# Performance work log

Measured on AMD Instinct MI355X. Metric: run time of the kernel, lower is better.

Reference implementation:

```python
import jax, jax.numpy as jnp
import numpy as np

N = 20000   # mesh vertices
B = 8       # batch
F = 64      # in_channels
K = 6       # Chebyshev order
OUT = 64    # out_channels
NNZ = 320000  # nonzeros in sparse Laplacian (avg degree 16)


def setup_inputs() -> dict:
    key = jax.random.key(0)
    ks = jax.random.split(key, 6)
    x = jax.random.normal(ks[0], (B, N, F), dtype=jnp.float32)
    lap_rows = jax.random.randint(ks[1], (NNZ,), 0, N, dtype=jnp.int32)
    lap_cols = jax.random.randint(ks[2], (NNZ,), 0, N, dtype=jnp.int32)
    lap_vals = jax.random.normal(ks[3], (NNZ,), dtype=jnp.float32) * 0.05
    # fc: Linear(K*F, OUT), xavier_normal weight, zero bias
    W = jax.random.normal(ks[4], (OUT, K * F), dtype=jnp.float32) * float(np.sqrt(2.0 / (K * F + OUT)))
    b = jnp.zeros((OUT,), dtype=jnp.float32)
    return {"x": x, "lap_rows": lap_rows, "lap_cols": lap_cols,
            "lap_vals": lap_vals, "W": W, "b": b}


def reference(x, lap_rows, lap_cols, lap_vals, W, b):
    Bd, Nd, Fd = x.shape

    def spmm(v):  # sparse [N,N] @ dense [N, B*F] via COO gather + segment_sum
        return jax.ops.segment_sum(lap_vals[:, None] * v[lap_cols], lap_rows,
                                   num_segments=Nd)

    x0 = jnp.transpose(x, (1, 0, 2)).reshape(Nd, Bd * Fd)  # [N, B*F]
    outs = [x0]
    if K > 1:
        tx1 = spmm(x0)
        outs.append(tx1)
        tx0 = x0
        for _ in range(2, K):  # Chebyshev recurrence T_k = 2 L T_{k-1} - T_{k-2}
            tx2 = 2.0 * spmm(tx1) - tx0
            outs.append(tx2)
            tx0, tx1 = tx1, tx2
    out = jnp.concatenate([o.reshape(Nd, Bd, Fd) for o in outs], axis=2)  # [N,B,K*F]
    out = out.reshape(Nd * Bd, K * Fd) @ W.T + b  # dense fc
    return jnp.transpose(out.reshape(Nd, Bd, -1), (1, 0, 2))  # [B,N,OUT]
```

## Files before the change

kernel.cpp:

```cpp
#include <hip/hip_runtime.h>

#define N_V  20000
#define B_   8
#define F_   64
#define K_   6
#define OUT_ 64
#define NNZ_ 320000
#define BF   512
#define NBUK N_V
#define SCANB 20
#define EPAD (NNZ_ + N_V * 7)

typedef unsigned short ushort_t;
typedef unsigned int   uint_t;

using frag_ab = __attribute__((ext_vector_type(8))) short;
using frag_cd = __attribute__((ext_vector_type(4))) float;

__device__ __forceinline__ ushort_t f2bf(float f) {
    uint_t u = __float_as_uint(f);
    u += 0x7FFFu + ((u >> 16) & 1u);
    return (ushort_t)(u >> 16);
}
__device__ __forceinline__ uint_t pack2(float lo, float hi) {
    return (uint_t)f2bf(lo) | ((uint_t)f2bf(hi) << 16);
}
__device__ __forceinline__ float bf2f(ushort_t u) {
    return __uint_as_float((uint_t)u << 16);
}


__global__ void hist_kernel(const int* __restrict__ rows, int* __restrict__ counts) {
    int e = blockIdx.x * 256 + threadIdx.x;
    if (e < NNZ_) atomicAdd(&counts[rows[e]], 1);
}

__global__ __launch_bounds__(1024) void scan1(const int* __restrict__ counts,
                                              int* __restrict__ incl, int* __restrict__ bsum) {
    __shared__ int buf[1024];
    int tid = threadIdx.x;
    int i = blockIdx.x * 1024 + tid;
    int c = (i < NBUK) ? ((counts[i] + 7) & ~7) : 0;
    buf[tid] = c;
    __syncthreads();
    for (int off = 1; off < 1024; off <<= 1) {
        int t = buf[tid];
        int add = (tid >= off) ? buf[tid - off] : 0;
        __syncthreads();
        buf[tid] = t + add;
        __syncthreads();
    }
    if (i < NBUK) incl[i] = buf[tid];
    if (tid == 1023) bsum[blockIdx.x] = buf[1023];
}

__global__ __launch_bounds__(256) void scan2(int* __restrict__ bsum) {
    __shared__ int buf[256];
    int tid = threadIdx.x;
    int c = (tid < SCANB) ? bsum[tid] : 0;
    buf[tid] = c;
    __syncthreads();
    for (int off = 1; off < 256; off <<= 1) {
        int t = buf[tid];
        int add = (tid >= off) ? buf[tid - off] : 0;
        __syncthreads();
        buf[tid] = t + add;
        __syncthreads();
    }
    if (tid < SCANB) bsum[tid] = buf[tid] - c;
}

__global__ __launch_bounds__(1024) void scan3(const int* __restrict__ counts,
                                              const int* __restrict__ bsum,
                                              int* __restrict__ bp, int* __restrict__ cursor) {
    int tid = threadIdx.x;
    int i = blockIdx.x * 1024 + tid;
    if (i < NBUK) {
        int pc = (counts[i] + 7) & ~7;
        int p = bsum[blockIdx.x] + cursor[i];
        bp[i + 1] = p;
        cursor[i] = p - pc;
    }
    if (i == 0) bp[0] = 0;
}

__global__ void scatter_kernel(const int* __restrict__ rows, const int* __restrict__ cols,
                               const float* __restrict__ vals, int* __restrict__ cursor,
                               int2* __restrict__ edges) {
    int e = blockIdx.x * 256 + threadIdx.x;
    if (e < NNZ_) {
        int pos = atomicAdd(&cursor[rows[e]], 1);
        edges[pos] = make_int2(cols[e], __float_as_int(vals[e]));
    }
}

__global__ void prep_kernel(const float* __restrict__ x, uint_t* __restrict__ X0,
                            const float* __restrict__ W, ushort_t* __restrict__ Wfrag) {
    int blk = blockIdx.x;
    if (blk < 20000) {
        int idx = blk * 256 + threadIdx.x;
        int f2 = idx & 31;
        int b  = (idx >> 5) & 7;
        int n  = idx >> 8;
        float2 v = *(const float2*)&x[((size_t)b * N_V + n) * F_ + f2 * 2];
        X0[n * 256 + b * 32 + f2] = pack2(v.x, v.y);
    } else {
        int idx = (blk - 20000) * 256 + threadIdx.x;
        if (idx < 12 * 4 * 64 * 8) {
            int j    = idx & 7;
            int lane = (idx >> 3) & 63;
            int ct   = (idx >> 9) & 3;
            int s    = idx >> 11;
            int o     = ct * 16 + (lane & 15);
            int kglob = s * 32 + ((lane >> 4) & 3) * 8 + j;
            Wfrag[idx] = f2bf(W[o * (K_ * F_) + kglob]);
        }
    }
}

template <bool RECUR>
__global__ __launch_bounds__(256) void cheb_row(const int* __restrict__ bp,
                                                const int2* __restrict__ edges,
                                                const ushort_t* __restrict__ Tprev,
                                                const ushort_t* __restrict__ Tpp,
                                                ushort_t* __restrict__ Tout) {
    const int wave = __builtin_amdgcn_readfirstlane(threadIdx.x >> 6);
    const int lane = threadIdx.x & 63;
    const int c    = blockIdx.x & 7;
    const int row  = ((blockIdx.x >> 3) << 2) + wave;

    const int st = bp[row];
    const int en = bp[row + 1];
    const ushort_t* Tp = Tprev + (c << 6) + lane;

    float a0 = 0.f, a1 = 0.f;
    for (int j = st; j < en; j += 8) {
        const int4* e4 = (const int4*)(edges + j);
        int4 E0 = e4[0], E1 = e4[1], E2 = e4[2], E3 = e4[3];
        const int c0 = __builtin_amdgcn_readfirstlane(E0.x);
        const int c1 = __builtin_amdgcn_readfirstlane(E0.z);
        const int c2 = __builtin_amdgcn_readfirstlane(E1.x);
        const int c3 = __builtin_amdgcn_readfirstlane(E1.z);
        const int c4 = __builtin_amdgcn_readfirstlane(E2.x);
        const int c5 = __builtin_amdgcn_readfirstlane(E2.z);
        const int c6 = __builtin_amdgcn_readfirstlane(E3.x);
        const int c7 = __builtin_amdgcn_readfirstlane(E3.z);
        const float v0 = __int_as_float(__builtin_amdgcn_readfirstlane(E0.y));
        const float v1 = __int_as_float(__builtin_amdgcn_readfirstlane(E0.w));
        const float v2 = __int_as_float(__builtin_amdgcn_readfirstlane(E1.y));
        const float v3 = __int_as_float(__builtin_amdgcn_readfirstlane(E1.w));
        const float v4 = __int_as_float(__builtin_amdgcn_readfirstlane(E2.y));
        const float v5 = __int_as_float(__builtin_amdgcn_readfirstlane(E2.w));
        const float v6 = __int_as_float(__builtin_amdgcn_readfirstlane(E3.y));
        const float v7 = __int_as_float(__builtin_amdgcn_readfirstlane(E3.w));

        ushort_t t0 = Tp[(size_t)c0 << 9];
        ushort_t t1 = Tp[(size_t)c1 << 9];
        ushort_t t2 = Tp[(size_t)c2 << 9];
        ushort_t t3 = Tp[(size_t)c3 << 9];
        ushort_t t4 = Tp[(size_t)c4 << 9];
        ushort_t t5 = Tp[(size_t)c5 << 9];
        ushort_t t6 = Tp[(size_t)c6 << 9];
        ushort_t t7 = Tp[(size_t)c7 << 9];

        a0 = fmaf(v0, bf2f(t0), a0);
        a1 = fmaf(v1, bf2f(t1), a1);
        a0 = fmaf(v2, bf2f(t2), a0);
        a1 = fmaf(v3, bf2f(t3), a1);
        a0 = fmaf(v4, bf2f(t4), a0);
        a1 = fmaf(v5, bf2f(t5), a1);
        a0 = fmaf(v6, bf2f(t6), a0);
        a1 = fmaf(v7, bf2f(t7), a1);
    }

    float res = a0 + a1;
    const size_t oidx = (size_t)row * BF + (c << 6) + lane;
    if (RECUR) {
        res = fmaf(2.f, res, -bf2f(Tpp[oidx]));
    }
    Tout[oidx] = f2bf(res);
}

__global__ __launch_bounds__(256) void fc_mfma(const ushort_t* __restrict__ X0,
                                               const ushort_t* __restrict__ T1,
                                               const ushort_t* __restrict__ T2,
                                               const ushort_t* __restrict__ T3,
                                               const ushort_t* __restrict__ T4,
                                               const ushort_t* __restrict__ T5,
                                               const ushort_t* __restrict__ Wfrag,
                                               const float* __restrict__ bias,
                                               float* __restrict__ out) {
    const int wave = threadIdx.x >> 6, lane = threadIdx.x & 63;
    const int quad = lane >> 4, col = lane & 15;
    const int tb = blockIdx.x * 128 + wave * 32;
    const int r0 = tb + col, r1 = tb + 16 + col;
    const ushort_t* Tbuf[6] = {X0, T1, T2, T3, T4, T5};

    frag_cd acc0[4], acc1[4];
#pragma unroll
    for (int ct = 0; ct < 4; ++ct) {
        acc0[ct] = (frag_cd){0.f, 0.f, 0.f, 0.f};
        acc1[ct] = (frag_cd){0.f, 0.f, 0.f, 0.f};
    }

#pragma unroll
    for (int s = 0; s < 12; ++s) {
        const int f0 = (s & 1) * 32 + quad * 8;
        frag_ab fa0 = *(const frag_ab*)(Tbuf[s >> 1] + (size_t)r0 * F_ + f0);
        frag_ab fa1 = *(const frag_ab*)(Tbuf[s >> 1] + (size_t)r1 * F_ + f0);
#pragma unroll
        for (int ct = 0; ct < 4; ++ct) {
            frag_ab bfr = *(const frag_ab*)(Wfrag + (((s * 4 + ct) * 64 + lane) << 3));
            acc0[ct] = __builtin_amdgcn_mfma_f32_16x16x32_bf16(fa0, bfr, acc0[ct], 0, 0, 0);
            acc1[ct] = __builtin_amdgcn_mfma_f32_16x16x32_bf16(fa1, bfr, acc1[ct], 0, 0, 0);
        }
    }

#pragma unroll
    for (int ct = 0; ct < 4; ++ct) {
        const int o = ct * 16 + col;
        const float bv = bias[o];
#pragma unroll
        for (int reg = 0; reg < 4; ++reg) {
            int ra = tb + quad * 4 + reg;
            int rb = ra + 16;
            out[(size_t)(ra & 7) * N_V * OUT_ + (size_t)(ra >> 3) * OUT_ + o] = acc0[ct][reg] + bv;
            out[(size_t)(rb & 7) * N_V * OUT_ + (size_t)(rb >> 3) * OUT_ + o] = acc1[ct][reg] + bv;
        }
    }
}


extern "C" void kernel_launch(void* const* d_in, const int* in_sizes, int n_in,
                              void* d_out, int out_size, void* d_ws, size_t ws_size,
                              hipStream_t stream) {
    const float* x    = (const float*)d_in[0];
    const int*   rows = (const int*)  d_in[1];
    const int*   cols = (const int*)  d_in[2];
    const float* vals = (const float*)d_in[3];
    const float* W    = (const float*)d_in[4];
    const float* bias = (const float*)d_in[5];
    float* out = (float*)d_out;

    const size_t TSZ = (size_t)N_V * BF;
    ushort_t* T1 = (ushort_t*)d_ws;
    ushort_t* T2 = T1 + TSZ;
    ushort_t* T3 = T2 + TSZ;
    ushort_t* T4 = T3 + TSZ;
    ushort_t* T5 = T4 + TSZ;
    ushort_t* X0 = T5 + TSZ;
    ushort_t* Wfrag = X0 + TSZ;
    int* counts    = (int*)(Wfrag + 24576);
    int* bp        = counts + NBUK;
    int* cursor    = bp + NBUK + 64;
    int* bsum      = cursor + NBUK;
    int2* edges    = (int2*)(bsum + 256);

    hipMemsetAsync(counts, 0, NBUK * sizeof(int), stream);
    hipMemsetAsync(edges, 0, (size_t)EPAD * sizeof(int2), stream);
    hist_kernel<<<(NNZ_ + 255) / 256, 256, 0, stream>>>(rows, counts);
    scan1<<<SCANB, 1024, 0, stream>>>(counts, cursor, bsum);
    scan2<<<1, 256, 0, stream>>>(bsum);
    scan3<<<SCANB, 1024, 0, stream>>>(counts, bsum, bp, cursor);
    scatter_kernel<<<(NNZ_ + 255) / 256, 256, 0, stream>>>(rows, cols, vals, cursor, edges);
    prep_kernel<<<20096, 256, 0, stream>>>(x, (uint_t*)X0, W, Wfrag);

    const int chebGrid = (N_V / 4) * 8;
    cheb_row<false><<<chebGrid, 256, 0, stream>>>(bp, edges, X0, nullptr, T1);
    cheb_row<true ><<<chebGrid, 256, 0, stream>>>(bp, edges, T1, X0, T2);
    cheb_row<true ><<<chebGrid, 256, 0, stream>>>(bp, edges, T2, T1, T3);
    cheb_row<true ><<<chebGrid, 256, 0, stream>>>(bp, edges, T3, T2, T4);
    cheb_row<true ><<<chebGrid, 256, 0, stream>>>(bp, edges, T4, T3, T5);

    fc_mfma<<<(N_V * B_) / 128, 256, 0, stream>>>(X0, T1, T2, T3, T4, T5, Wfrag, bias, out);
}
```

Before: 453.0 us.

## Process two rows per wave with 4-wide feature vectors and edge-group split

Rewrites the Chebyshev SpMM kernel so each wave handles two adjacent rows. Lanes are split into 4 edge groups of 16 lanes, and each lane loads 4 bf16 features (8 bytes) per gathered neighbor instead of one 2-byte value. Per-row edge padding rises from 8 to 16 so a 16-edge step stays within the padded region, and partial sums are reduced across groups with shuffles. The aim is wider gather loads and fewer waves, at the cost of more zero padding work, extra padded-edge memory and a cross-lane reduction.

```diff
diff --git a/kernel.cpp b/kernel.cpp
--- a/kernel.cpp
+++ b/kernel.cpp
@@ -9,7 +9,7 @@
 #define BF   512
 #define NBUK N_V
 #define SCANB 20
-#define EPAD (NNZ_ + N_V * 7)
+#define EPAD (NNZ_ + N_V * 15)
 
 typedef unsigned short ushort_t;
 typedef unsigned int   uint_t;
@@ -25,8 +25,9 @@
 __device__ __forceinline__ uint_t pack2(float lo, float hi) {
     return (uint_t)f2bf(lo) | ((uint_t)f2bf(hi) << 16);
 }
-__device__ __forceinline__ float bf2f(ushort_t u) {
-    return __uint_as_float((uint_t)u << 16);
+__device__ __forceinline__ void unpack2(uint_t u, float& lo, float& hi) {
+    lo = __uint_as_float(u << 16);
+    hi = __uint_as_float(u & 0xFFFF0000u);
 }
 
 
@@ -40,7 +41,7 @@
     __shared__ int buf[1024];
     int tid = threadIdx.x;
     int i = blockIdx.x * 1024 + tid;
-    int c = (i < NBUK) ? ((counts[i] + 7) & ~7) : 0;
+    int c = (i < NBUK) ? ((counts[i] + 15) & ~15) : 0;
     buf[tid] = c;
     __syncthreads();
     for (int off = 1; off < 1024; off <<= 1) {
@@ -76,7 +77,7 @@
     int tid = threadIdx.x;
     int i = blockIdx.x * 1024 + tid;
     if (i < NBUK) {
-        int pc = (counts[i] + 7) & ~7;
+        int pc = (counts[i] + 15) & ~15;
         int p = bsum[blockIdx.x] + cursor[i];
         bp[i + 1] = p;
         cursor[i] = p - pc;
@@ -119,66 +120,99 @@
 }
 
 template <bool RECUR>
-__global__ __launch_bounds__(256) void cheb_row(const int* __restrict__ bp,
-                                                const int2* __restrict__ edges,
-                                                const ushort_t* __restrict__ Tprev,
-                                                const ushort_t* __restrict__ Tpp,
-                                                ushort_t* __restrict__ Tout) {
-    const int wave = __builtin_amdgcn_readfirstlane(threadIdx.x >> 6);
-    const int lane = threadIdx.x & 63;
+__global__ __launch_bounds__(256) void cheb_row2(const int* __restrict__ bp,
+                                                 const int2* __restrict__ edges,
+                                                 const ushort_t* __restrict__ Tprev,
+                                                 const ushort_t* __restrict__ Tpp,
+                                                 ushort_t* __restrict__ Tout) {
+    const int wave = threadIdx.x >> 6, lane = threadIdx.x & 63;
     const int c    = blockIdx.x & 7;
-    const int row  = ((blockIdx.x >> 3) << 2) + wave;
-
-    const int st = bp[row];
-    const int en = bp[row + 1];
-    const ushort_t* Tp = Tprev + (c << 6) + lane;
-
-    float a0 = 0.f, a1 = 0.f;
-    for (int j = st; j < en; j += 8) {
-        const int4* e4 = (const int4*)(edges + j);
-        int4 E0 = e4[0], E1 = e4[1], E2 = e4[2], E3 = e4[3];
-        const int c0 = __builtin_amdgcn_readfirstlane(E0.x);
-        const int c1 = __builtin_amdgcn_readfirstlane(E0.z);
-        const int c2 = __builtin_amdgcn_readfirstlane(E1.x);
-        const int c3 = __builtin_amdgcn_readfirstlane(E1.z);
-        const int c4 = __builtin_amdgcn_readfirstlane(E2.x);
-        const int c5 = __builtin_amdgcn_readfirstlane(E2.z);
-        const int c6 = __builtin_amdgcn_readfirstlane(E3.x);
-        const int c7 = __builtin_amdgcn_readfirstlane(E3.z);
-        const float v0 = __int_as_float(__builtin_amdgcn_readfirstlane(E0.y));
-        const float v1 = __int_as_float(__builtin_amdgcn_readfirstlane(E0.w));
-        const float v2 = __int_as_float(__builtin_amdgcn_readfirstlane(E1.y));
-        const float v3 = __int_as_float(__builtin_amdgcn_readfirstlane(E1.w));
-        const float v4 = __int_as_float(__builtin_amdgcn_readfirstlane(E2.y));
-        const float v5 = __int_as_float(__builtin_amdgcn_readfirstlane(E2.w));
-        const float v6 = __int_as_float(__builtin_amdgcn_readfirstlane(E3.y));
-        const float v7 = __int_as_float(__builtin_amdgcn_readfirstlane(E3.w));
-
-        ushort_t t0 = Tp[(size_t)c0 << 9];
-        ushort_t t1 = Tp[(size_t)c1 << 9];
-        ushort_t t2 = Tp[(size_t)c2 << 9];
-        ushort_t t3 = Tp[(size_t)c3 << 9];
-        ushort_t t4 = Tp[(size_t)c4 << 9];
-        ushort_t t5 = Tp[(size_t)c5 << 9];
-        ushort_t t6 = Tp[(size_t)c6 << 9];
-        ushort_t t7 = Tp[(size_t)c7 << 9];
-
-        a0 = fmaf(v0, bf2f(t0), a0);
-        a1 = fmaf(v1, bf2f(t1), a1);
-        a0 = fmaf(v2, bf2f(t2), a0);
-        a1 = fmaf(v3, bf2f(t3), a1);
-        a0 = fmaf(v4, bf2f(t4), a0);
-        a1 = fmaf(v5, bf2f(t5), a1);
-        a0 = fmaf(v6, bf2f(t6), a0);
-        a1 = fmaf(v7, bf2f(t7), a1);
-    }
-
-    float res = a0 + a1;
-    const size_t oidx = (size_t)row * BF + (c << 6) + lane;
-    if (RECUR) {
-        res = fmaf(2.f, res, -bf2f(Tpp[oidx]));
-    }
-    Tout[oidx] = f2bf(res);
+    const int pair = (blockIdx.x >> 3) * 4 + wave;
+    const int r0   = pair * 2;
+    const int g    = lane >> 4;
+    const int f4   = (lane & 15) << 2;
+
+    const int st  = bp[r0];
+    const int mid = bp[r0 + 1];
+    const int en  = bp[r0 + 2];
+
+    const ushort_t* Tb = Tprev + (c << 6) + f4;
+    const int2*    eb  = edges + g * 4;
+
+    float a0 = 0.f, a1 = 0.f, a2 = 0.f, a3 = 0.f;
+    float b0 = 0.f, b1 = 0.f, b2 = 0.f, b3 = 0.f;
+
+    for (int j = st; j < en; j += 16) {
+        const int4* ep = (const int4*)(eb + j);
+        int4 Ea = ep[0];
+        int4 Eb = ep[1];
+        uint2 u0 = *(const uint2*)(Tb + ((size_t)Ea.x << 9));
+        uint2 u1 = *(const uint2*)(Tb + ((size_t)Ea.z << 9));
+        uint2 u2 = *(const uint2*)(Tb + ((size_t)Eb.x << 9));
+        uint2 u3 = *(const uint2*)(Tb + ((size_t)Eb.z << 9));
+        const float v0 = __int_as_float(Ea.y);
+        const float v1 = __int_as_float(Ea.w);
+        const float v2 = __int_as_float(Eb.y);
+        const float v3 = __int_as_float(Eb.w);
+        float e0, e1, e2, e3;
+        if (j < mid) {
+            unpack2(u0.x, e0, e1); unpack2(u0.y, e2, e3);
+            a0 = fmaf(v0, e0, a0); a1 = fmaf(v0, e1, a1);
+            a2 = fmaf(v0, e2, a2); a3 = fmaf(v0, e3, a3);
+            unpack2(u1.x, e0, e1); unpack2(u1.y, e2, e3);
+            a0 = fmaf(v1, e0, a0); a1 = fmaf(v1, e1, a1);
+            a2 = fmaf(v1, e2, a2); a3 = fmaf(v1, e3, a3);
+            unpack2(u2.x, e0, e1); unpack2(u2.y, e2, e3);
+            a0 = fmaf(v2, e0, a0); a1 = fmaf(v2, e1, a1);
+            a2 = fmaf(v2, e2, a2); a3 = fmaf(v2, e3, a3);
+            unpack2(u3.x, e0, e1); unpack2(u3.y, e2, e3);
+            a0 = fmaf(v3, e0, a0); a1 = fmaf(v3, e1, a1);
+            a2 = fmaf(v3, e2, a2); a3 = fmaf(v3, e3, a3);
+        } else {
+            unpack2(u0.x, e0, e1); unpack2(u0.y, e2, e3);
+            b0 = fmaf(v0, e0, b0); b1 = fmaf(v0, e1, b1);
+            b2 = fmaf(v0, e2, b2); b3 = fmaf(v0, e3, b3);
+            unpack2(u1.x, e0, e1); unpack2(u1.y, e2, e3);
+            b0 = fmaf(v1, e0, b0); b1 = fmaf(v1, e1, b1);
+            b2 = fmaf(v1, e2, b2); b3 = fmaf(v1, e3, b3);
+            unpack2(u2.x, e0, e1); unpack2(u2.y, e2, e3);
+            b0 = fmaf(v2, e0, b0); b1 = fmaf(v2, e1, b1);
+            b2 = fmaf(v2, e2, b2); b3 = fmaf(v2, e3, b3);
+            unpack2(u3.x, e0, e1); unpack2(u3.y, e2, e3);
+            b0 = fmaf(v3, e0, b0); b1 = fmaf(v3, e1, b1);
+            b2 = fmaf(v3, e2, b2); b3 = fmaf(v3, e3, b3);
+        }
+    }
+
+    a0 += __shfl_xor(a0, 16, 64); a0 += __shfl_xor(a0, 32, 64);
+    a1 += __shfl_xor(a1, 16, 64); a1 += __shfl_xor(a1, 32, 64);
+    a2 += __shfl_xor(a2, 16, 64); a2 += __shfl_xor(a2, 32, 64);
+    a3 += __shfl_xor(a3, 16, 64); a3 += __shfl_xor(a3, 32, 64);
+    b0 += __shfl_xor(b0, 16, 64); b0 += __shfl_xor(b0, 32, 64);
+    b1 += __shfl_xor(b1, 16, 64); b1 += __shfl_xor(b1, 32, 64);
+    b2 += __shfl_xor(b2, 16, 64); b2 += __shfl_xor(b2, 32, 64);
+    b3 += __shfl_xor(b3, 16, 64); b3 += __shfl_xor(b3, 32, 64);
+
+    if (lane < 32) {
+        float s0 = (lane < 16) ? a0 : b0;
+        float s1 = (lane < 16) ? a1 : b1;
+        float s2 = (lane < 16) ? a2 : b2;
+        float s3 = (lane < 16) ? a3 : b3;
+        const size_t o = (size_t)(r0 + (lane >> 4)) * BF + (c << 6) + f4;
+        if (RECUR) {
+            uint2 up = *(const uint2*)(Tpp + o);
+            float p0, p1, p2, p3;
+            unpack2(up.x, p0, p1); unpack2(up.y, p2, p3);
+            s0 = fmaf(2.f, s0, -p0);
+            s1 = fmaf(2.f, s1, -p1);
+            s2 = fmaf(2.f, s2, -p2);
+            s3 = fmaf(2.f, s3, -p3);
+        }
+        uint2 st2;
+        st2.x = pack2(s0, s1);
+        st2.y = pack2(s2, s3);
+        *(uint2*)(Tout + o) = st2;
+    }
 }
 
 __global__ __launch_bounds__(256) void fc_mfma(const ushort_t* __restrict__ X0,
@@ -265,12 +299,12 @@
     scatter_kernel<<<(NNZ_ + 255) / 256, 256, 0, stream>>>(rows, cols, vals, cursor, edges);
     prep_kernel<<<20096, 256, 0, stream>>>(x, (uint_t*)X0, W, Wfrag);
 
-    const int chebGrid = (N_V / 4) * 8;
-    cheb_row<false><<<chebGrid, 256, 0, stream>>>(bp, edges, X0, nullptr, T1);
-    cheb_row<true ><<<chebGrid, 256, 0, stream>>>(bp, edges, T1, X0, T2);
-    cheb_row<true ><<<chebGrid, 256, 0, stream>>>(bp, edges, T2, T1, T3);
-    cheb_row<true ><<<chebGrid, 256, 0, stream>>>(bp, edges, T3, T2, T4);
-    cheb_row<true ><<<chebGrid, 256, 0, stream>>>(bp, edges, T4, T3, T5);
+    const int chebGrid = 2500 * 8;
+    cheb_row2<false><<<chebGrid, 256, 0, stream>>>(bp, edges, X0, nullptr, T1);
+    cheb_row2<true ><<<chebGrid, 256, 0, stream>>>(bp, edges, T1, X0, T2);
+    cheb_row2<true ><<<chebGrid, 256, 0, stream>>>(bp, edges, T2, T1, T3);
+    cheb_row2<true ><<<chebGrid, 256, 0, stream>>>(bp, edges, T3, T2, T4);
+    cheb_row2<true ><<<chebGrid, 256, 0, stream>>>(bp, edges, T4, T3, T5);
 
     fc_mfma<<<(N_V * B_) / 128, 256, 0, stream>>>(X0, T1, T2, T3, T4, T5, Wfrag, bias, out);
 }
```

New measurement: 420.3 us. 7.2% less time.

## Restructure Chebyshev SpMM: wave handles two rows with 8-edge lanes and 16-byte gathers

Applied to the files above, without the earlier changes.

Rewrites the sparse Chebyshev step so each wave covers two adjacent rows of a 64-column chunk. The 64 lanes are split into 8 edge slots of 8 lanes, and each lane gathers 8 bf16 features with a single 16-byte load instead of one 2-byte load per lane. Edge and gather loads are software-pipelined two iterations ahead, and partial sums are combined with cross-lane shuffles before 16 lanes write vectorized outputs. This targets the small scalar gathers and per-edge uniform-register broadcasts, at the cost of extra shuffle reductions and per-edge row-select branching.

```diff
diff --git a/kernel.cpp b/kernel.cpp
--- a/kernel.cpp
+++ b/kernel.cpp
@@ -25,8 +25,9 @@
 __device__ __forceinline__ uint_t pack2(float lo, float hi) {
     return (uint_t)f2bf(lo) | ((uint_t)f2bf(hi) << 16);
 }
-__device__ __forceinline__ float bf2f(ushort_t u) {
-    return __uint_as_float((uint_t)u << 16);
+__device__ __forceinline__ void unpack2(uint_t u, float& lo, float& hi) {
+    lo = __uint_as_float(u << 16);
+    hi = __uint_as_float(u & 0xFFFF0000u);
 }
 
 
@@ -119,66 +120,95 @@
 }
 
 template <bool RECUR>
-__global__ __launch_bounds__(256) void cheb_row(const int* __restrict__ bp,
-                                                const int2* __restrict__ edges,
-                                                const ushort_t* __restrict__ Tprev,
-                                                const ushort_t* __restrict__ Tpp,
-                                                ushort_t* __restrict__ Tout) {
-    const int wave = __builtin_amdgcn_readfirstlane(threadIdx.x >> 6);
-    const int lane = threadIdx.x & 63;
+__global__ __launch_bounds__(256) void cheb_row8(const int* __restrict__ bp,
+                                                 const int2* __restrict__ edges,
+                                                 const ushort_t* __restrict__ Tprev,
+                                                 const ushort_t* __restrict__ Tpp,
+                                                 ushort_t* __restrict__ Tout) {
+    const int wave = threadIdx.x >> 6, lane = threadIdx.x & 63;
     const int c    = blockIdx.x & 7;
-    const int row  = ((blockIdx.x >> 3) << 2) + wave;
-
-    const int st = bp[row];
-    const int en = bp[row + 1];
-    const ushort_t* Tp = Tprev + (c << 6) + lane;
-
-    float a0 = 0.f, a1 = 0.f;
-    for (int j = st; j < en; j += 8) {
-        const int4* e4 = (const int4*)(edges + j);
-        int4 E0 = e4[0], E1 = e4[1], E2 = e4[2], E3 = e4[3];
-        const int c0 = __builtin_amdgcn_readfirstlane(E0.x);
-        const int c1 = __builtin_amdgcn_readfirstlane(E0.z);
-        const int c2 = __builtin_amdgcn_readfirstlane(E1.x);
-        const int c3 = __builtin_amdgcn_readfirstlane(E1.z);
-        const int c4 = __builtin_amdgcn_readfirstlane(E2.x);
-        const int c5 = __builtin_amdgcn_readfirstlane(E2.z);
-        const int c6 = __builtin_amdgcn_readfirstlane(E3.x);
-        const int c7 = __builtin_amdgcn_readfirstlane(E3.z);
-        const float v0 = __int_as_float(__builtin_amdgcn_readfirstlane(E0.y));
-        const float v1 = __int_as_float(__builtin_amdgcn_readfirstlane(E0.w));
-        const float v2 = __int_as_float(__builtin_amdgcn_readfirstlane(E1.y));
-        const float v3 = __int_as_float(__builtin_amdgcn_readfirstlane(E1.w));
-        const float v4 = __int_as_float(__builtin_amdgcn_readfirstlane(E2.y));
-        const float v5 = __int_as_float(__builtin_amdgcn_readfirstlane(E2.w));
-        const float v6 = __int_as_float(__builtin_amdgcn_readfirstlane(E3.y));
-        const float v7 = __int_as_float(__builtin_amdgcn_readfirstlane(E3.w));
-
-        ushort_t t0 = Tp[(size_t)c0 << 9];
-        ushort_t t1 = Tp[(size_t)c1 << 9];
-        ushort_t t2 = Tp[(size_t)c2 << 9];
-        ushort_t t3 = Tp[(size_t)c3 << 9];
-        ushort_t t4 = Tp[(size_t)c4 << 9];
-        ushort_t t5 = Tp[(size_t)c5 << 9];
-        ushort_t t6 = Tp[(size_t)c6 << 9];
-        ushort_t t7 = Tp[(size_t)c7 << 9];
-
-        a0 = fmaf(v0, bf2f(t0), a0);
-        a1 = fmaf(v1, bf2f(t1), a1);
-        a0 = fmaf(v2, bf2f(t2), a0);
-        a1 = fmaf(v3, bf2f(t3), a1);
-        a0 = fmaf(v4, bf2f(t4), a0);
-        a1 = fmaf(v5, bf2f(t5), a1);
-        a0 = fmaf(v6, bf2f(t6), a0);
-        a1 = fmaf(v7, bf2f(t7), a1);
-    }
-
-    float res = a0 + a1;
-    const size_t oidx = (size_t)row * BF + (c << 6) + lane;
-    if (RECUR) {
-        res = fmaf(2.f, res, -bf2f(Tpp[oidx]));
-    }
-    Tout[oidx] = f2bf(res);
+    const int pair = (blockIdx.x >> 3) * 4 + wave;
+    const int r0   = pair * 2;
+    const int sub  = lane >> 3;
+    const int f8   = (lane & 7) << 3;
+
+    const int st  = bp[r0];
+    const int mid = bp[r0 + 1];
+    const int en  = bp[r0 + 2];
+
+    const ushort_t* Tb = Tprev + (c << 6) + f8;
+    const int2*    eb  = edges + sub;
+
+    float aA0 = 0.f, aA1 = 0.f, aA2 = 0.f, aA3 = 0.f,
+          aA4 = 0.f, aA5 = 0.f, aA6 = 0.f, aA7 = 0.f;
+    float aB0 = 0.f, aB1 = 0.f, aB2 = 0.f, aB3 = 0.f,
+          aB4 = 0.f, aB5 = 0.f, aB6 = 0.f, aB7 = 0.f;
+
+    if (st < en) {
+        const int lim = en - 8;
+        int2 E0 = eb[st];
+        int2 E1 = eb[min(st + 8, lim)];
+        int2 E2 = eb[min(st + 16, lim)];
+        uint4 G0 = *(const uint4*)(Tb + ((size_t)(uint_t)E0.x << 9));
+        uint4 G1 = *(const uint4*)(Tb + ((size_t)(uint_t)E1.x << 9));
+        float v0 = __int_as_float(E0.y);
+        float v1 = __int_as_float(E1.y);
+
+        for (int j = st; j < en; j += 8) {
+            uint4 Gn = *(const uint4*)(Tb + ((size_t)(uint_t)E2.x << 9));
+            float vn = __int_as_float(E2.y);
+            int2 En = eb[min(j + 24, lim)];
+            float e0, e1, e2, e3, e4, e5, e6, e7;
+            unpack2(G0.x, e0, e1); unpack2(G0.y, e2, e3);
+            unpack2(G0.z, e4, e5); unpack2(G0.w, e6, e7);
+            if (j < mid) {
+                aA0 = fmaf(v0, e0, aA0); aA1 = fmaf(v0, e1, aA1);
+                aA2 = fmaf(v0, e2, aA2); aA3 = fmaf(v0, e3, aA3);
+                aA4 = fmaf(v0, e4, aA4); aA5 = fmaf(v0, e5, aA5);
+                aA6 = fmaf(v0, e6, aA6); aA7 = fmaf(v0, e7, aA7);
+            } else {
+                aB0 = fmaf(v0, e0, aB0); aB1 = fmaf(v0, e1, aB1);
+                aB2 = fmaf(v0, e2, aB2); aB3 = fmaf(v0, e3, aB3);
+                aB4 = fmaf(v0, e4, aB4); aB5 = fmaf(v0, e5, aB5);
+                aB6 = fmaf(v0, e6, aB6); aB7 = fmaf(v0, e7, aB7);
+            }
+            G0 = G1; v0 = v1; G1 = Gn; v1 = vn; E2 = En;
+        }
+    }
+
+#define RED(x) x += __shfl_xor(x, 8, 64); x += __shfl_xor(x, 16, 64); x += __shfl_xor(x, 32, 64)
+    RED(aA0); RED(aA1); RED(aA2); RED(aA3); RED(aA4); RED(aA5); RED(aA6); RED(aA7);
+    RED(aB0); RED(aB1); RED(aB2); RED(aB3); RED(aB4); RED(aB5); RED(aB6); RED(aB7);
+#undef RED
+
+    if (lane < 16) {
+        const int isB = lane >> 3;
+        float s0 = isB ? aB0 : aA0;
+        float s1 = isB ? aB1 : aA1;
+        float s2 = isB ? aB2 : aA2;
+        float s3 = isB ? aB3 : aA3;
+        float s4 = isB ? aB4 : aA4;
+        float s5 = isB ? aB5 : aA5;
+        float s6 = isB ? aB6 : aA6;
+        float s7 = isB ? aB7 : aA7;
+        const size_t o = (size_t)(r0 + isB) * BF + (c << 6) + f8;
+        if (RECUR) {
+            uint4 up = *(const uint4*)(Tpp + o);
+            float p0, p1, p2, p3, p4, p5, p6, p7;
+            unpack2(up.x, p0, p1); unpack2(up.y, p2, p3);
+            unpack2(up.z, p4, p5); unpack2(up.w, p6, p7);
+            s0 = fmaf(2.f, s0, -p0); s1 = fmaf(2.f, s1, -p1);
+            s2 = fmaf(2.f, s2, -p2); s3 = fmaf(2.f, s3, -p3);
+            s4 = fmaf(2.f, s4, -p4); s5 = fmaf(2.f, s5, -p5);
+            s6 = fmaf(2.f, s6, -p6); s7 = fmaf(2.f, s7, -p7);
+        }
+        uint4 st4;
+        st4.x = pack2(s0, s1);
+        st4.y = pack2(s2, s3);
+        st4.z = pack2(s4, s5);
+        st4.w = pack2(s6, s7);
+        *(uint4*)(Tout + o) = st4;
+    }
 }
 
 __global__ __launch_bounds__(256) void fc_mfma(const ushort_t* __restrict__ X0,
@@ -265,12 +295,12 @@
     scatter_kernel<<<(NNZ_ + 255) / 256, 256, 0, stream>>>(rows, cols, vals, cursor, edges);
     prep_kernel<<<20096, 256, 0, stream>>>(x, (uint_t*)X0, W, Wfrag);
 
-    const int chebGrid = (N_V / 4) * 8;
-    cheb_row<false><<<chebGrid, 256, 0, stream>>>(bp, edges, X0, nullptr, T1);
-    cheb_row<true ><<<chebGrid, 256, 0, stream>>>(bp, edges, T1, X0, T2);
-    cheb_row<true ><<<chebGrid, 256, 0, stream>>>(bp, edges, T2, T1, T3);
-    cheb_row<true ><<<chebGrid, 256, 0, stream>>>(bp, edges, T3, T2, T4);
-    cheb_row<true ><<<chebGrid, 256, 0, stream>>>(bp, edges, T4, T3, T5);
+    const int chebGrid = 2500 * 8;
+    cheb_row8<false><<<chebGrid, 256, 0, stream>>>(bp, edges, X0, nullptr, T1);
+    cheb_row8<true ><<<chebGrid, 256, 0, stream>>>(bp, edges, T1, X0, T2);
+    cheb_row8<true ><<<chebGrid, 256, 0, stream>>>(bp, edges, T2, T1, T3);
+    cheb_row8<true ><<<chebGrid, 256, 0, stream>>>(bp, edges, T3, T2, T4);
+    cheb_row8<true ><<<chebGrid, 256, 0, stream>>>(bp, edges, T4, T3, T5);
 
     fc_mfma<<<(N_V * B_) / 128, 256, 0, stream>>>(X0, T1, T2, T3, T4, T5, Wfrag, bias, out);
 }
```

Result: faster. 423.5 us (-6.5%).

## Restructure Chebyshev SpMM to 16-byte gathers over row pairs, merge scan kernels

Applied to the files above, without the earlier changes.

The SpMM kernel now has each wave handle four rows as two pairs. Its 8 edge-subgroups each gather 16-byte bf16 vectors, with prefetch of the next edges and gathers. Cross-lane shuffle reductions combine the subgroup sums. This replaces the old scheme of one 2-byte gather per lane per edge, and aims to raise memory-level parallelism and cut instruction count per edge. The three scan kernels are merged into a single-block scan, and the two memsets are merged into one. The cost is more registers, shuffle overhead, and load imbalance between paired rows.

```diff
diff --git a/kernel.cpp b/kernel.cpp
--- a/kernel.cpp
+++ b/kernel.cpp
@@ -8,7 +8,6 @@
 #define NNZ_ 320000
 #define BF   512
 #define NBUK N_V
-#define SCANB 20
 #define EPAD (NNZ_ + N_V * 7)
 
 typedef unsigned short ushort_t;
@@ -25,8 +24,9 @@
 __device__ __forceinline__ uint_t pack2(float lo, float hi) {
     return (uint_t)f2bf(lo) | ((uint_t)f2bf(hi) << 16);
 }
-__device__ __forceinline__ float bf2f(ushort_t u) {
-    return __uint_as_float((uint_t)u << 16);
+__device__ __forceinline__ void unpack2(uint_t u, float& lo, float& hi) {
+    lo = __uint_as_float(u << 16);
+    hi = __uint_as_float(u & 0xFFFF0000u);
 }
 
 
@@ -35,13 +35,22 @@
     if (e < NNZ_) atomicAdd(&counts[rows[e]], 1);
 }
 
-__global__ __launch_bounds__(1024) void scan1(const int* __restrict__ counts,
-                                              int* __restrict__ incl, int* __restrict__ bsum) {
+__global__ __launch_bounds__(1024) void scan_all(const int* __restrict__ counts,
+                                                 int* __restrict__ bp,
+                                                 int* __restrict__ cursor) {
     __shared__ int buf[1024];
-    int tid = threadIdx.x;
-    int i = blockIdx.x * 1024 + tid;
-    int c = (i < NBUK) ? ((counts[i] + 7) & ~7) : 0;
-    buf[tid] = c;
+    const int tid = threadIdx.x;
+    int loc[20];
+    int s = 0;
+    if (tid < 1000) {
+        const int base = tid * 20;
+#pragma unroll
+        for (int k = 0; k < 20; ++k) {
+            loc[k] = s;
+            s += (counts[base + k] + 7) & ~7;
+        }
+    }
+    buf[tid] = s;
     __syncthreads();
     for (int off = 1; off < 1024; off <<= 1) {
         int t = buf[tid];
@@ -50,38 +59,17 @@
         buf[tid] = t + add;
         __syncthreads();
     }
-    if (i < NBUK) incl[i] = buf[tid];
-    if (tid == 1023) bsum[blockIdx.x] = buf[1023];
-}
-
-__global__ __launch_bounds__(256) void scan2(int* __restrict__ bsum) {
-    __shared__ int buf[256];
-    int tid = threadIdx.x;
-    int c = (tid < SCANB) ? bsum[tid] : 0;
-    buf[tid] = c;
-    __syncthreads();
-    for (int off = 1; off < 256; off <<= 1) {
-        int t = buf[tid];
-        int add = (tid >= off) ? buf[tid - off] : 0;
-        __syncthreads();
-        buf[tid] = t + add;
-        __syncthreads();
-    }
-    if (tid < SCANB) bsum[tid] = buf[tid] - c;
-}
-
-__global__ __launch_bounds__(1024) void scan3(const int* __restrict__ counts,
-                                              const int* __restrict__ bsum,
-                                              int* __restrict__ bp, int* __restrict__ cursor) {
-    int tid = threadIdx.x;
-    int i = blockIdx.x * 1024 + tid;
-    if (i < NBUK) {
-        int pc = (counts[i] + 7) & ~7;
-        int p = bsum[blockIdx.x] + cursor[i];
-        bp[i + 1] = p;
-        cursor[i] = p - pc;
-    }
-    if (i == 0) bp[0] = 0;
+    const int excl = buf[tid] - s;
+    if (tid < 1000) {
+        const int base = tid * 20;
+#pragma unroll
+        for (int k = 0; k < 20; ++k) {
+            const int p = excl + loc[k];
+            bp[base + k] = p;
+            cursor[base + k] = p;
+        }
+    }
+    if (tid == 1023) bp[NBUK] = buf[1023];
 }
 
 __global__ void scatter_kernel(const int* __restrict__ rows, const int* __restrict__ cols,
@@ -118,67 +106,123 @@
     }
 }
 
+#define CONS(Gv, vv, isA, accA, accB)                                          \
+    {                                                                          \
+        float e_[8];                                                           \
+        unpack2(Gv.x, e_[0], e_[1]); unpack2(Gv.y, e_[2], e_[3]);              \
+        unpack2(Gv.z, e_[4], e_[5]); unpack2(Gv.w, e_[6], e_[7]);              \
+        if (isA) {                                                             \
+            _Pragma("unroll")                                                  \
+            for (int i_ = 0; i_ < 8; ++i_) accA[i_] = fmaf(vv, e_[i_], accA[i_]); \
+        } else {                                                               \
+            _Pragma("unroll")                                                  \
+            for (int i_ = 0; i_ < 8; ++i_) accB[i_] = fmaf(vv, e_[i_], accB[i_]); \
+        }                                                                      \
+    }
+
 template <bool RECUR>
-__global__ __launch_bounds__(256) void cheb_row(const int* __restrict__ bp,
-                                                const int2* __restrict__ edges,
-                                                const ushort_t* __restrict__ Tprev,
-                                                const ushort_t* __restrict__ Tpp,
-                                                ushort_t* __restrict__ Tout) {
-    const int wave = __builtin_amdgcn_readfirstlane(threadIdx.x >> 6);
-    const int lane = threadIdx.x & 63;
+__global__ __launch_bounds__(256) void cheb_quad(const int* __restrict__ bp,
+                                                 const int2* __restrict__ edges,
+                                                 const ushort_t* __restrict__ Tprev,
+                                                 const ushort_t* __restrict__ Tpp,
+                                                 ushort_t* __restrict__ Tout) {
+    const int wave = threadIdx.x >> 6, lane = threadIdx.x & 63;
     const int c    = blockIdx.x & 7;
-    const int row  = ((blockIdx.x >> 3) << 2) + wave;
-
-    const int st = bp[row];
-    const int en = bp[row + 1];
-    const ushort_t* Tp = Tprev + (c << 6) + lane;
-
-    float a0 = 0.f, a1 = 0.f;
-    for (int j = st; j < en; j += 8) {
-        const int4* e4 = (const int4*)(edges + j);
-        int4 E0 = e4[0], E1 = e4[1], E2 = e4[2], E3 = e4[3];
-        const int c0 = __builtin_amdgcn_readfirstlane(E0.x);
-        const int c1 = __builtin_amdgcn_readfirstlane(E0.z);
-        const int c2 = __builtin_amdgcn_readfirstlane(E1.x);
-        const int c3 = __builtin_amdgcn_readfirstlane(E1.z);
-        const int c4 = __builtin_amdgcn_readfirstlane(E2.x);
-        const int c5 = __builtin_amdgcn_readfirstlane(E2.z);
-        const int c6 = __builtin_amdgcn_readfirstlane(E3.x);
-        const int c7 = __builtin_amdgcn_readfirstlane(E3.z);
-        const float v0 = __int_as_float(__builtin_amdgcn_readfirstlane(E0.y));
-        const float v1 = __int_as_float(__builtin_amdgcn_readfirstlane(E0.w));
-        const float v2 = __int_as_float(__builtin_amdgcn_readfirstlane(E1.y));
-        const float v3 = __int_as_float(__builtin_amdgcn_readfirstlane(E1.w));
-        const float v4 = __int_as_float(__builtin_amdgcn_readfirstlane(E2.y));
-        const float v5 = __int_as_float(__builtin_amdgcn_readfirstlane(E2.w));
-        const float v6 = __int_as_float(__builtin_amdgcn_readfirstlane(E3.y));
-        const float v7 = __int_as_float(__builtin_amdgcn_readfirstlane(E3.w));
-
-        ushort_t t0 = Tp[(size_t)c0 << 9];
-        ushort_t t1 = Tp[(size_t)c1 << 9];
-        ushort_t t2 = Tp[(size_t)c2 << 9];
-        ushort_t t3 = Tp[(size_t)c3 << 9];
-        ushort_t t4 = Tp[(size_t)c4 << 9];
-        ushort_t t5 = Tp[(size_t)c5 << 9];
-        ushort_t t6 = Tp[(size_t)c6 << 9];
-        ushort_t t7 = Tp[(size_t)c7 << 9];
-
-        a0 = fmaf(v0, bf2f(t0), a0);
-        a1 = fmaf(v1, bf2f(t1), a1);
-        a0 = fmaf(v2, bf2f(t2), a0);
-        a1 = fmaf(v3, bf2f(t3), a1);
-        a0 = fmaf(v4, bf2f(t4), a0);
-        a1 = fmaf(v5, bf2f(t5), a1);
-        a0 = fmaf(v6, bf2f(t6), a0);
-        a1 = fmaf(v7, bf2f(t7), a1);
-    }
-
-    float res = a0 + a1;
-    const size_t oidx = (size_t)row * BF + (c << 6) + lane;
-    if (RECUR) {
-        res = fmaf(2.f, res, -bf2f(Tpp[oidx]));
-    }
-    Tout[oidx] = f2bf(res);
+    const int grp  = (blockIdx.x >> 3) * 4 + wave;
+    const int r0   = grp * 4;
+    const int sub  = lane >> 3;
+    const int f8   = (lane & 7) << 3;
+
+    int bpv = bp[r0 + min(lane, 4)];
+    const int st0  = __builtin_amdgcn_readfirstlane(__shfl(bpv, 0, 64));
+    const int mid0 = __builtin_amdgcn_readfirstlane(__shfl(bpv, 1, 64));
+    const int en0  = __builtin_amdgcn_readfirstlane(__shfl(bpv, 2, 64));
+    const int mid1 = __builtin_amdgcn_readfirstlane(__shfl(bpv, 3, 64));
+    const int en1  = __builtin_amdgcn_readfirstlane(__shfl(bpv, 4, 64));
+    const int st1  = en0;
+
+    const int n0 = (en0 - st0) >> 3;
+    const int n1 = (en1 - st1) >> 3;
+    const int maxit = max(n0, n1);
+
+    const ushort_t* Tb = Tprev + (c << 6) + f8;
+    const int2*     eb = edges + sub;
+
+    float accA0[8], accB0[8], accA1[8], accB1[8];
+#pragma unroll
+    for (int i = 0; i < 8; ++i) { accA0[i] = 0.f; accB0[i] = 0.f; accA1[i] = 0.f; accB1[i] = 0.f; }
+
+    if (maxit > 0) {
+        const int safe0 = (n0 > 0) ? st0 : 0;
+        const int safe1 = (n1 > 0) ? st1 : 0;
+        const int last0 = safe0 + 8 * (max(n0, 1) - 1);
+        const int last1 = safe1 + 8 * (max(n1, 1) - 1);
+
+        int a0 = safe0, a1 = safe1;
+        int2 E0a = eb[a0];
+        int2 E1a = eb[a1];
+        int2 E0n = eb[min(safe0 + 8, last0)];
+        int2 E1n = eb[min(safe1 + 8, last1)];
+        uint4 G0 = *(const uint4*)(Tb + ((size_t)(uint_t)E0a.x << 9));
+        uint4 G1 = *(const uint4*)(Tb + ((size_t)(uint_t)E1a.x << 9));
+        float v0 = (n0 > 0) ? __int_as_float(E0a.y) : 0.f;
+        float v1 = (n1 > 0) ? __int_as_float(E1a.y) : 0.f;
+
+        for (int it = 0; it < maxit; ++it) {
+            uint4 Gn0 = *(const uint4*)(Tb + ((size_t)(uint_t)E0n.x << 9));
+            uint4 Gn1 = *(const uint4*)(Tb + ((size_t)(uint_t)E1n.x << 9));
+            const float vn0 = (it + 1 < n0) ? __int_as_float(E0n.y) : 0.f;
+            const float vn1 = (it + 1 < n1) ? __int_as_float(E1n.y) : 0.f;
+            int2 E0t = eb[min(a0 + 16, last0)];
+            int2 E1t = eb[min(a1 + 16, last1)];
+            CONS(G0, v0, (a0 < mid0), accA0, accB0);
+            CONS(G1, v1, (a1 < mid1), accA1, accB1);
+            G0 = Gn0; v0 = vn0; G1 = Gn1; v1 = vn1;
+            E0n = E0t; E1n = E1t;
+            a0 = min(a0 + 8, last0);
+            a1 = min(a1 + 8, last1);
+        }
+    }
+
+#pragma unroll
+    for (int i = 0; i < 8; ++i) {
+        accA0[i] += __shfl_xor(accA0[i], 8, 64); accA0[i] += __shfl_xor(accA0[i], 16, 64); accA0[i] += __shfl_xor(accA0[i], 32, 64);
+        accB0[i] += __shfl_xor(accB0[i], 8, 64); accB0[i] += __shfl_xor(accB0[i], 16, 64); accB0[i] += __shfl_xor(accB0[i], 32, 64);
+        accA1[i] += __shfl_xor(accA1[i], 8, 64); accA1[i] += __shfl_xor(accA1[i], 16, 64); accA1[i] += __shfl_xor(accA1[i], 32, 64);
+        accB1[i] += __shfl_xor(accB1[i], 8, 64); accB1[i] += __shfl_xor(accB1[i], 16, 64); accB1[i] += __shfl_xor(accB1[i], 32, 64);
+    }
+
+    if (lane < 16) {
+        const int isB = lane >> 3;
+        float s0[8], s1[8];
+#pragma unroll
+        for (int i = 0; i < 8; ++i) {
+            s0[i] = isB ? accB0[i] : accA0[i];
+            s1[i] = isB ? accB1[i] : accA1[i];
+        }
+        const size_t o0 = (size_t)(r0 + isB)     * BF + (c << 6) + f8;
+        const size_t o1 = (size_t)(r0 + 2 + isB) * BF + (c << 6) + f8;
+        if (RECUR) {
+            uint4 up0 = *(const uint4*)(Tpp + o0);
+            uint4 up1 = *(const uint4*)(Tpp + o1);
+            float p[8];
+            unpack2(up0.x, p[0], p[1]); unpack2(up0.y, p[2], p[3]);
+            unpack2(up0.z, p[4], p[5]); unpack2(up0.w, p[6], p[7]);
+#pragma unroll
+            for (int i = 0; i < 8; ++i) s0[i] = fmaf(2.f, s0[i], -p[i]);
+            unpack2(up1.x, p[0], p[1]); unpack2(up1.y, p[2], p[3]);
+            unpack2(up1.z, p[4], p[5]); unpack2(up1.w, p[6], p[7]);
+#pragma unroll
+            for (int i = 0; i < 8; ++i) s1[i] = fmaf(2.f, s1[i], -p[i]);
+        }
+        uint4 w0, w1;
+        w0.x = pack2(s0[0], s0[1]); w0.y = pack2(s0[2], s0[3]);
+        w0.z = pack2(s0[4], s0[5]); w0.w = pack2(s0[6], s0[7]);
+        w1.x = pack2(s1[0], s1[1]); w1.y = pack2(s1[2], s1[3]);
+        w1.z = pack2(s1[4], s1[5]); w1.w = pack2(s1[6], s1[7]);
+        *(uint4*)(Tout + o0) = w0;
+        *(uint4*)(Tout + o1) = w1;
+    }
 }
 
 __global__ __launch_bounds__(256) void fc_mfma(const ushort_t* __restrict__ X0,
@@ -250,27 +294,23 @@
     ushort_t* T5 = T4 + TSZ;
     ushort_t* X0 = T5 + TSZ;
     ushort_t* Wfrag = X0 + TSZ;
-    int* counts    = (int*)(Wfrag + 24576);
-    int* bp        = counts + NBUK;
-    int* cursor    = bp + NBUK + 64;
-    int* bsum      = cursor + NBUK;
-    int2* edges    = (int2*)(bsum + 256);
-
-    hipMemsetAsync(counts, 0, NBUK * sizeof(int), stream);
-    hipMemsetAsync(edges, 0, (size_t)EPAD * sizeof(int2), stream);
+    int*  counts = (int*)(Wfrag + 24576);
+    int2* edges  = (int2*)(counts + NBUK);
+    int*  bp     = (int*)(edges + EPAD);
+    int*  cursor = bp + NBUK + 64;
+
+    hipMemsetAsync(counts, 0, NBUK * sizeof(int) + (size_t)EPAD * sizeof(int2), stream);
     hist_kernel<<<(NNZ_ + 255) / 256, 256, 0, stream>>>(rows, counts);
-    scan1<<<SCANB, 1024, 0, stream>>>(counts, cursor, bsum);
-    scan2<<<1, 256, 0, stream>>>(bsum);
-    scan3<<<SCANB, 1024, 0, stream>>>(counts, bsum, bp, cursor);
+    scan_all<<<1, 1024, 0, stream>>>(counts, bp, cursor);
     scatter_kernel<<<(NNZ_ + 255) / 256, 256, 0, stream>>>(rows, cols, vals, cursor, edges);
     prep_kernel<<<20096, 256, 0, stream>>>(x, (uint_t*)X0, W, Wfrag);
 
-    const int chebGrid = (N_V / 4) * 8;
-    cheb_row<false><<<chebGrid, 256, 0, stream>>>(bp, edges, X0, nullptr, T1);
-    cheb_row<true ><<<chebGrid, 256, 0, stream>>>(bp, edges, T1, X0, T2);
-    cheb_row<true ><<<chebGrid, 256, 0, stream>>>(bp, edges, T2, T1, T3);
-    cheb_row<true ><<<chebGrid, 256, 0, stream>>>(bp, edges, T3, T2, T4);
-    cheb_row<true ><<<chebGrid, 256, 0, stream>>>(bp, edges, T4, T3, T5);
+    const int chebGrid = 1250 * 8;
+    cheb_quad<false><<<chebGrid, 256, 0, stream>>>(bp, edges, X0, nullptr, T1);
+    cheb_quad<true ><<<chebGrid, 256, 0, stream>>>(bp, edges, T1, X0, T2);
+    cheb_quad<true ><<<chebGrid, 256, 0, stream>>>(bp, edges, T2, T1, T3);
+    cheb_quad<true ><<<chebGrid, 256, 0, stream>>>(bp, edges, T3, T2, T4);
+    cheb_quad<true ><<<chebGrid, 256, 0, stream>>>(bp, edges, T4, T3, T5);
 
     fc_mfma<<<(N_V * B_) / 128, 256, 0, stream>>>(X0, T1, T2, T3, T4, T5, Wfrag, bias, out);
 }
```

New measurement: 444.5 us. No clear change (-1.9%).
